# Performance work log

Measured on AMD Instinct MI355X. Metric: run time of the kernel, lower is better.

Reference implementation:

```python
import jax, jax.numpy as jnp
import numpy as np

N, IN_DIM, HID = 8192, 256, 512
NEG_INF = jnp.float32(-1e30)


def _linear_params(key, fan_in, fan_out):
    k1, k2 = jax.random.split(key)
    bound = 1.0 / np.sqrt(fan_in)
    W = jax.random.uniform(k1, (fan_in, fan_out), jnp.float32, -bound, bound)
    b = jax.random.uniform(k2, (fan_out,), jnp.float32, -bound, bound)
    return W, b


def setup_inputs() -> dict:
    key = jax.random.key(0)
    ks = jax.random.split(key, 10)
    x = jax.random.normal(ks[0], (N, IN_DIM), jnp.float32)
    adj = jax.random.randint(ks[1], (N, N), 0, 2) > 0
    adj = adj | jnp.eye(N, dtype=bool)  # self-loops: no all-masked rows
    Win, b_in = _linear_params(ks[2], IN_DIM, HID)
    Wq, bq = _linear_params(ks[3], HID, HID)
    Wk, bk = _linear_params(ks[4], HID, HID)
    Wv, bv = _linear_params(ks[5], HID, HID)
    Wo, bo = _linear_params(ks[6], HID, HID)
    Ws, bs = _linear_params(ks[7], HID, 1)
    Wf1, bf1 = _linear_params(ks[8], HID, HID)
    Wf2, bf2 = _linear_params(ks[9], HID, HID)
    g1 = jnp.ones((HID,), jnp.float32); be1 = jnp.zeros((HID,), jnp.float32)
    g2 = jnp.ones((HID,), jnp.float32); be2 = jnp.zeros((HID,), jnp.float32)
    return dict(x=x, adj=adj, Win=Win, b_in=b_in, Wq=Wq, bq=bq, Wk=Wk, bk=bk,
                Wv=Wv, bv=bv, Wo=Wo, bo=bo, Ws=Ws, bs=bs,
                g1=g1, be1=be1, g2=g2, be2=be2,
                Wf1=Wf1, bf1=bf1, Wf2=Wf2, bf2=bf2)


def _layernorm(x, g, b, eps=1e-5):
    mu = jnp.mean(x, axis=-1, keepdims=True)
    var = jnp.mean(jnp.square(x - mu), axis=-1, keepdims=True)
    return (x - mu) * jax.lax.rsqrt(var + eps) * g + b


def reference(x, adj, Win, b_in, Wq, bq, Wk, bk, Wv, bv, Wo, bo, Ws, bs,
              g1, be1, g2, be2, Wf1, bf1, Wf2, bf2):
    h = x @ Win + b_in                      # [N, HID]
    q = h @ Wq + bq
    k = h @ Wk + bk
    v = h @ Wv + bv
    scale = 1.0 / np.sqrt(HID).astype(np.float32)
    scores = (q @ k.T) * scale              # [N, N]
    scores = jnp.where(adj, scores, NEG_INF)
    attn = jax.nn.softmax(scores, axis=-1)  # dropout = identity (eval mode)
    h2 = attn @ v                           # [N, HID]
    h = _layernorm(h + (h2 @ Wo + bo), g1, be1)
    ff = jnp.maximum(h @ Wf1 + bf1, 0.0) @ Wf2 + bf2
    h = _layernorm(h + ff, g2, be2)
    logits = (h @ Ws + bs).squeeze(-1)      # [N]
    return logits
```

## Files before the change

### kernel.cpp

```cpp
#include <hip/hip_runtime.h>

typedef unsigned int u32;
typedef unsigned short u16;
typedef unsigned char u8;

typedef __bf16 bf16_t;
typedef bf16_t bf16x8 __attribute__((ext_vector_type(8)));
typedef float f32x4 __attribute__((ext_vector_type(4)));

#define NROW 8192
#define HID 512
#define DIN 256
#define LDQ 1536
#define NSPLIT 4
#define KVCH (NROW / NSPLIT)
#define KVB 32

__device__ __forceinline__ u16 f2b(float f) {
    u32 u = __float_as_uint(f);
    u32 r = (u + 0x7fffu + ((u >> 16) & 1u)) >> 16;
    return (u16)r;
}
__device__ __forceinline__ float b2f(u16 h) {
    return __uint_as_float(((u32)h) << 16);
}
__device__ __forceinline__ f32x4 zero4() {
    f32x4 z = {0.f, 0.f, 0.f, 0.f};
    return z;
}
__device__ __forceinline__ void gll16(const void* g, void* l) {
    __builtin_amdgcn_global_load_lds(
        (const __attribute__((address_space(1))) unsigned int*)g,
        (__attribute__((address_space(3))) unsigned int*)l, 16, 0, 0);
}

__global__ void sniff_and_bias(const u32* __restrict__ adj, int* __restrict__ mode,
                               const float* __restrict__ bq, const float* __restrict__ bk,
                               const float* __restrict__ bv, float* __restrict__ bqkv) {
    __shared__ int f01[4], ff32[4], fbf[4];
    int t = threadIdx.x, lane = t & 63, wv = t >> 6;
    for (int i = t; i < 1536; i += 256)
        bqkv[i] = i < 512 ? bq[i] : (i < 1024 ? bk[i - 512] : bv[i - 1024]);
    int all01 = 1, allf32 = 1, allbf = 1;
    for (int i = t; i < 1024; i += 256) {
        u32 w = adj[i];
        if (w > 1u) all01 = 0;
        if (w != 0u && w != 0x3f800000u) allf32 = 0;
    }
    const u16* h = (const u16*)adj;
    for (int i = t; i < 2048; i += 256) {
        u16 v = h[i];
        if (v != 0 && v != 0x3f80u) allbf = 0;
    }
    all01 = __all(all01);
    allf32 = __all(allf32);
    allbf = __all(allbf);
    if (lane == 0) { f01[wv] = all01; ff32[wv] = allf32; fbf[wv] = allbf; }
    __syncthreads();
    if (t == 0) {
        int a = f01[0] & f01[1] & f01[2] & f01[3];
        int b = ff32[0] & ff32[1] & ff32[2] & ff32[3];
        int c = fbf[0] & fbf[1] & fbf[2] & fbf[3];
        mode[0] = a ? 0 : (b ? 1 : (c ? 2 : 3));
    }
}

__global__ __launch_bounds__(256) void build_bits(const void* __restrict__ adj,
                                                  const int* __restrict__ mode,
                                                  u32* __restrict__ bits) {
    int row = blockIdx.x;
    int t = threadIdx.x;
    int lane = t & 63, wv = t >> 6;
    int md = *mode;
    for (int c0 = 0; c0 < NROW; c0 += 256) {
        int c = c0 + t;
        size_t idx = (size_t)row * NROW + c;
        bool nz;
        if (md == 0)      nz = ((const u32*)adj)[idx] != 0u;
        else if (md == 1) nz = ((const float*)adj)[idx] != 0.f;
        else if (md == 2) nz = ((const u16*)adj)[idx] != 0;
        else              nz = ((const u8*)adj)[idx] != 0;
        unsigned long long bm = __ballot(nz);
        if (lane == 0) {
            int w = row * 256 + (c0 >> 5) + wv * 2;
            bits[w] = (u32)bm;
            bits[w + 1] = (u32)(bm >> 32);
        }
    }
}

__global__ __launch_bounds__(256) void prep(const float* __restrict__ x,
                                            const float* __restrict__ Win,
                                            const float* __restrict__ Wq,
                                            const float* __restrict__ Wk,
                                            const float* __restrict__ Wv,
                                            const float* __restrict__ Wo,
                                            const float* __restrict__ Wf1,
                                            const float* __restrict__ Wf2,
                                            u16* __restrict__ pX16,
                                            u16* __restrict__ pWinT,
                                            u16* __restrict__ pQKVT,
                                            u16* __restrict__ pWoT,
                                            u16* __restrict__ pWf1T,
                                            u16* __restrict__ pWf2T) {
    int z = blockIdx.z;
    int t = threadIdx.x;
    if (z == 7) {
        size_t base = ((size_t)blockIdx.y * 8 + blockIdx.x) * 32768;
#pragma unroll 4
        for (int k = 0; k < 128; k++) {
            size_t i = base + k * 256 + t;
            pX16[i] = f2b(x[i]);
        }
        return;
    }
    const float* src;
    u16* dst;
    int R = 512;
    switch (z) {
        case 0: src = Win; dst = pWinT; R = 256; break;
        case 1: src = Wq;  dst = pQKVT; break;
        case 2: src = Wk;  dst = pQKVT + 512 * 512; break;
        case 3: src = Wv;  dst = pQKVT + 2 * 512 * 512; break;
        case 4: src = Wo;  dst = pWoT; break;
        case 5: src = Wf1; dst = pWf1T; break;
        default: src = Wf2; dst = pWf2T; break;
    }
    int r0 = blockIdx.y * 64, c0 = blockIdx.x * 64;
    if (r0 >= R) return;
    __shared__ u16 tile[64][65];
#pragma unroll
    for (int i = 0; i < 16; i++) {
        int idx = t + i * 256;
        int rr = idx >> 6, cc = idx & 63;
        tile[rr][cc] = f2b(src[(size_t)(r0 + rr) * 512 + c0 + cc]);
    }
    __syncthreads();
#pragma unroll
    for (int i = 0; i < 16; i++) {
        int idx = t + i * 256;
        int rr = idx >> 6, cc = idx & 63;
        dst[(size_t)(c0 + rr) * R + r0 + cc] = tile[cc][rr];
    }
}

__global__ __launch_bounds__(256) void transpose_v_tiled(const u16* __restrict__ in, int ldv,
                                                         u16* __restrict__ out) {
    __shared__ u16 tl[64][72];
    int c0 = blockIdx.x * 64;
    int r0 = blockIdx.y * 64;
    int t = threadIdx.x;
#pragma unroll
    for (int i = 0; i < 2; i++) {
        int idx = t + i * 256;
        int rr = idx >> 3, ck = idx & 7;
        bf16x8 v = *(const bf16x8*)(in + (size_t)(r0 + rr) * ldv + c0 + ck * 8);
#pragma unroll
        for (int j = 0; j < 8; j++) tl[ck * 8 + j][rr] = ((u16*)&v)[j];
    }
    __syncthreads();
#pragma unroll
    for (int i = 0; i < 2; i++) {
        int idx = t + i * 256;
        int col = idx >> 3, ch = idx & 7;
        int kv = ch * 8;
        bf16x8 v;
#pragma unroll
        for (int j = 0; j < 8; j++) ((u16*)&v)[j] = tl[col][kv + j];
        *(bf16x8*)(out + (size_t)((r0 + kv) >> 5) * (HID * 32) +
                   (size_t)(c0 + col) * 32 + (kv & 31)) = v;
    }
}

__global__ __launch_bounds__(256, 3) void gemm_k(const u16* __restrict__ A, int lda,
                                                 const u16* __restrict__ Bt,
                                                 const float* __restrict__ bias,
                                                 const float* __restrict__ resid,
                                                 float* __restrict__ outF,
                                                 u16* __restrict__ outH, int ldo,
                                                 int relu, int K) {
    __shared__ u16 Ald[2][8192];
    __shared__ u16 Bld[2][4096];
    int t = threadIdx.x;
    int lane = t & 63, wave = t >> 6;
    int l15 = lane & 15, lg = lane >> 4;
    int row0 = blockIdx.y * 128, col0 = blockIdx.x * 64;

    auto stage = [&](int buf, int kk) {
#pragma unroll
        for (int p = 0; p < 4; p++) {
            int idx = p * 256 + t;
            int row = idx >> 3, c = idx & 7;
            gll16(A + (size_t)(row0 + row) * lda + kk + ((c ^ (row & 7)) * 8),
                  &Ald[buf][idx * 8]);
        }
#pragma unroll
        for (int p = 0; p < 2; p++) {
            int idx = p * 256 + t;
            int row = idx >> 3, c = idx & 7;
            gll16(Bt + (size_t)(col0 + row) * K + kk + ((c ^ (row & 7)) * 8),
                  &Bld[buf][idx * 8]);
        }
    };

    f32x4 acc[2][4];
#pragma unroll
    for (int i = 0; i < 2; i++)
#pragma unroll
        for (int j = 0; j < 4; j++) acc[i][j] = zero4();

    stage(0, 0);
    asm volatile("s_waitcnt vmcnt(0)" ::: "memory");
    __syncthreads();

    int nk = K >> 6;
    for (int kt = 0; kt < nk; kt++) {
        int buf = kt & 1;
        if (kt + 1 < nk) stage(buf ^ 1, (kt + 1) * 64);
#pragma unroll
        for (int ks = 0; ks < 2; ks++) {
            bf16x8 af[2], bfr[4];
#pragma unroll
            for (int i = 0; i < 2; i++) {
                int row = wave * 32 + i * 16 + l15;
                af[i] = *(const bf16x8*)&Ald[buf][row * 64 + (((ks * 4 + lg) ^ (row & 7)) * 8)];
            }
#pragma unroll
            for (int j = 0; j < 4; j++) {
                int row = j * 16 + l15;
                bfr[j] = *(const bf16x8*)&Bld[buf][row * 64 + (((ks * 4 + lg) ^ (row & 7)) * 8)];
            }
            __builtin_amdgcn_s_setprio(1);
#pragma unroll
            for (int i = 0; i < 2; i++)
#pragma unroll
                for (int j = 0; j < 4; j++)
                    acc[i][j] = __builtin_amdgcn_mfma_f32_16x16x32_bf16(af[i], bfr[j],
                                                                       acc[i][j], 0, 0, 0);
            __builtin_amdgcn_s_setprio(0);
        }
        asm volatile("s_waitcnt vmcnt(0)" ::: "memory");
        __syncthreads();
    }
#pragma unroll
    for (int j = 0; j < 4; j++) {
        int col = col0 + j * 16 + l15;
        float bv = bias[col];
#pragma unroll
        for (int i = 0; i < 2; i++) {
#pragma unroll
            for (int r = 0; r < 4; r++) {
                int row = row0 + wave * 32 + i * 16 + lg * 4 + r;
                float v = acc[i][j][r] + bv;
                if (relu) v = fmaxf(v, 0.f);
                size_t o = (size_t)row * ldo + col;
                if (resid) v += resid[o];
                if (outF) outF[o] = v;
                if (outH) outH[o] = f2b(v);
            }
        }
    }
}

__global__ __launch_bounds__(512, 2) void attn_kernel(const u16* __restrict__ QKV,
                                                      const u16* __restrict__ VTt,
                                                      const u32* __restrict__ bits,
                                                      u16* __restrict__ Opart,
                                                      float* __restrict__ Mpart,
                                                      float* __restrict__ Lpart) {
    extern __shared__ char smem[];
    u16* Klds = (u16*)smem;
    u16* Plds = (u16*)(smem + 98304);
    float* cscL = (float*)(smem + 114688);
    int* flagsL = (int*)(smem + 115712);
    int lane = threadIdx.x & 63, wave = threadIdx.x >> 6;
    int l15 = lane & 15, lg = lane >> 4;
    int s = blockIdx.x & 3;
    int qb = blockIdx.x >> 2;
    int qrow0 = qb * 128;
    int myrows = qrow0 + wave * 16;
    const u16* Kg = QKV + 512;

    bf16x8 qf[16];
    {
        const u16* qp = QKV + (size_t)(myrows + l15) * LDQ + lg * 8;
#pragma unroll
        for (int ks = 0; ks < 16; ks++) qf[ks] = *(const bf16x8*)(qp + ks * 32);
    }

    f32x4 acc[8][4];
#pragma unroll
    for (int i = 0; i < 8; i++)
#pragma unroll
        for (int j = 0; j < 4; j++) acc[i][j] = zero4();
    float m[4] = {-1e30f, -1e30f, -1e30f, -1e30f};
    float lsum[4] = {0.f, 0.f, 0.f, 0.f};
    const float scale = 0.04419417382415922f;
    int kvbeg = s * KVCH;

    auto STAGE = [&](int buf, int kv0) {
#pragma unroll
        for (int i = 0; i < 4; i++) {
            int seg = wave * 4 + i;
            int ks = seg >> 1, q = seg & 1;
            gll16(Kg + (size_t)(kv0 + q * 16 + l15) * LDQ + ks * 32 + lg * 8,
                  Klds + buf * 16384 + seg * 512 + lane * 8);
        }
    };

    STAGE(0, kvbeg);
    STAGE(1, kvbeg + KVB);
    asm volatile("s_waitcnt vmcnt(4)" ::: "memory");
    __builtin_amdgcn_sched_barrier(0);
    __builtin_amdgcn_s_barrier();
    __builtin_amdgcn_sched_barrier(0);

    const int NT = KVCH / KVB;
    for (int t = 0; t < NT; ++t) {
        int kv0 = kvbeg + t * KVB;
        const u16* kb = Klds + (t % 3) * 16384;
        int pb = t & 1;

        f32x4 sf[2];
        sf[0] = zero4(); sf[1] = zero4();
        __builtin_amdgcn_s_setprio(1);
#pragma unroll
        for (int ks = 0; ks < 16; ks++) {
            bf16x8 b0 = *(const bf16x8*)(kb + (ks * 2) * 512 + lane * 8);
            bf16x8 b1 = *(const bf16x8*)(kb + (ks * 2 + 1) * 512 + lane * 8);
            sf[0] = __builtin_amdgcn_mfma_f32_16x16x32_bf16(qf[ks], b0, sf[0], 0, 0, 0);
            sf[1] = __builtin_amdgcn_mfma_f32_16x16x32_bf16(qf[ks], b1, sf[1], 0, 0, 0);
        }
        __builtin_amdgcn_s_setprio(0);

        u32 w0[4];
#pragma unroll
        for (int r = 0; r < 4; r++)
            w0[r] = bits[(size_t)(myrows + lg * 4 + r) * 256 + (kv0 >> 5)];
        float pvv[2][4];
        float mx[4] = {-1e30f, -1e30f, -1e30f, -1e30f};
#pragma unroll
        for (int f = 0; f < 2; f++) {
            int c = f * 16 + l15;
#pragma unroll
            for (int r = 0; r < 4; r++) {
                bool bit = (w0[r] >> c) & 1u;
                float sv = bit ? sf[f][r] * scale : -1e30f;
                pvv[f][r] = sv;
                mx[r] = fmaxf(mx[r], sv);
            }
        }
        bool need = false;
#pragma unroll
        for (int r = 0; r < 4; r++) need |= (mx[r] > m[r] + 8.0f);
        int wneed = __any(need ? 1 : 0);
        float cscv[4] = {1.f, 1.f, 1.f, 1.f};
        if (wneed) {
#pragma unroll
            for (int r = 0; r < 4; r++) {
#pragma unroll
                for (int off = 8; off; off >>= 1)
                    mx[r] = fmaxf(mx[r], __shfl_xor(mx[r], off, 64));
                float mn = fmaxf(m[r], mx[r]);
                cscv[r] = __expf(m[r] - mn);
                m[r] = mn;
                lsum[r] *= cscv[r];
            }
        }
        if (l15 == 0) *(f32x4*)&cscL[pb * 128 + wave * 16 + lg * 4] = *(f32x4*)cscv;
        if (lane == 0) flagsL[pb * 8 + wave] = wneed;

#pragma unroll
        for (int f = 0; f < 2; f++)
#pragma unroll
            for (int r = 0; r < 4; r++)
                pvv[f][r] = (pvv[f][r] < -1e29f) ? 0.f : __expf(pvv[f][r] - m[r]);
#pragma unroll
        for (int r = 0; r < 4; r++)
            lsum[r] += pvv[0][r] + pvv[1][r];

#pragma unroll
        for (int f = 0; f < 2; f++)
#pragma unroll
            for (int r = 0; r < 4; r++)
                Plds[pb * 4096 + wave * 512 + (f * 2 + (l15 >> 3)) * 128 +
                     (lg * 4 + r) * 8 + (l15 & 7)] = f2b(pvv[f][r]);

        const u16* vb = VTt + (size_t)(kv0 >> 5) * (HID * 32) + (size_t)(wave * 64) * 32;
        bf16x8 vv[4];
#pragma unroll
        for (int c4 = 0; c4 < 4; c4++)
            vv[c4] = *(const bf16x8*)(vb + (size_t)(c4 * 16 + l15) * 32 + lg * 8);

        if (t + 2 < NT) {
            STAGE((t + 2) % 3, kv0 + 2 * KVB);
            asm volatile("s_waitcnt vmcnt(4)" ::: "memory");
        } else if (t + 1 < NT) {
            asm volatile("s_waitcnt vmcnt(0)" ::: "memory");
        }
        asm volatile("s_waitcnt lgkmcnt(0)" ::: "memory");
        __builtin_amdgcn_sched_barrier(0);
        __builtin_amdgcn_s_barrier();
        __builtin_amdgcn_sched_barrier(0);

        int anyf = __any(flagsL[pb * 8 + (lane & 7)] != 0);
        if (anyf) {
#pragma unroll
            for (int rf = 0; rf < 8; rf++) {
                f32x4 cs = *(const f32x4*)&cscL[pb * 128 + rf * 16 + lg * 4];
#pragma unroll
                for (int cf = 0; cf < 4; cf++) {
                    f32x4 a = acc[rf][cf];
                    a[0] *= cs[0]; a[1] *= cs[1]; a[2] *= cs[2]; a[3] *= cs[3];
                    acc[rf][cf] = a;
                }
            }
        }

        __builtin_amdgcn_s_setprio(1);
#pragma unroll
        for (int rf = 0; rf < 8; rf++) {
            bf16x8 pa = *(const bf16x8*)(Plds + pb * 4096 + rf * 512 + lane * 8);
#pragma unroll
            for (int cf = 0; cf < 4; cf++)
                acc[rf][cf] = __builtin_amdgcn_mfma_f32_16x16x32_bf16(pa, vv[cf],
                                                                     acc[rf][cf], 0, 0, 0);
        }
        __builtin_amdgcn_s_setprio(0);
    }

#pragma unroll
    for (int r = 0; r < 4; r++) {
#pragma unroll
        for (int off = 8; off; off >>= 1)
            lsum[r] += __shfl_xor(lsum[r], off, 64);
    }
    if (l15 == 0) {
#pragma unroll
        for (int r = 0; r < 4; r++) {
            size_t o = (size_t)s * NROW + myrows + lg * 4 + r;
            Mpart[o] = m[r];
            Lpart[o] = lsum[r];
        }
    }
#pragma unroll
    for (int rf = 0; rf < 8; rf++)
#pragma unroll
        for (int cf = 0; cf < 4; cf++) {
            int col = wave * 64 + cf * 16 + l15;
#pragma unroll
            for (int j = 0; j < 4; j++) {
                size_t row = (size_t)s * NROW + qrow0 + rf * 16 + lg * 4 + j;
                Opart[row * HID + col] = f2b(acc[rf][cf][j]);
            }
        }
}

__global__ __launch_bounds__(256) void attn_combine(const u16* __restrict__ Opart,
                                                    const float* __restrict__ Mpart,
                                                    const float* __restrict__ Lpart,
                                                    u16* __restrict__ O16) {
    int idx = blockIdx.x * 256 + threadIdx.x;
    int row = idx >> 6;
    int c8 = (idx & 63) << 3;
    float ms[NSPLIT], M = -1e30f;
#pragma unroll
    for (int s = 0; s < NSPLIT; s++) {
        ms[s] = Mpart[(size_t)s * NROW + row];
        M = fmaxf(M, ms[s]);
    }
    float w[NSPLIT], L = 0.f;
#pragma unroll
    for (int s = 0; s < NSPLIT; s++) {
        w[s] = __expf(ms[s] - M);
        L += Lpart[(size_t)s * NROW + row] * w[s];
    }
    float inv = 1.f / L;
    float o[8];
#pragma unroll
    for (int j = 0; j < 8; j++) o[j] = 0.f;
#pragma unroll
    for (int s = 0; s < NSPLIT; s++) {
        bf16x8 p = *(const bf16x8*)(Opart + ((size_t)s * NROW + row) * HID + c8);
#pragma unroll
        for (int j = 0; j < 8; j++) o[j] += (float)p[j] * w[s];
    }
    bf16x8 res;
#pragma unroll
    for (int j = 0; j < 8; j++) {
        u16 b = f2b(o[j] * inv);
        res[j] = *(bf16_t*)&b;
    }
    *(bf16x8*)(O16 + (size_t)row * HID + c8) = res;
}

__global__ __launch_bounds__(256) void ln_single(const float* __restrict__ a,
                                                 const float* __restrict__ g,
                                                 const float* __restrict__ be,
                                                 float* __restrict__ outF,
                                                 u16* __restrict__ outH) {
    int row = blockIdx.x, t = threadIdx.x;
    const float* ar = a + (size_t)row * HID;
    float x0 = ar[t];
    float x1 = ar[t + 256];
    float s = x0 + x1, s2 = x0 * x0 + x1 * x1;
#pragma unroll
    for (int off = 32; off; off >>= 1) {
        s += __shfl_xor(s, off, 64);
        s2 += __shfl_xor(s2, off, 64);
    }
    __shared__ float ls[4], ls2[4];
    int wv = t >> 6, ln = t & 63;
    if (ln == 0) { ls[wv] = s; ls2[wv] = s2; }
    __syncthreads();
    float S = ls[0] + ls[1] + ls[2] + ls[3];
    float S2 = ls2[0] + ls2[1] + ls2[2] + ls2[3];
    float mu = S * (1.f / 512.f);
    float var = S2 * (1.f / 512.f) - mu * mu;
    float inv = rsqrtf(var + 1e-5f);
    float y0 = (x0 - mu) * inv * g[t] + be[t];
    float y1 = (x1 - mu) * inv * g[t + 256] + be[t + 256];
    size_t o = (size_t)row * HID + t;
    outF[o] = y0; outF[o + 256] = y1;
    outH[o] = f2b(y0); outH[o + 256] = f2b(y1);
}

__global__ __launch_bounds__(256) void ln_logits(const float* __restrict__ a,
                                                 const float* __restrict__ g,
                                                 const float* __restrict__ be,
                                                 const float* __restrict__ Ws,
                                                 const float* __restrict__ bs,
                                                 float* __restrict__ out) {
    int row = blockIdx.x, t = threadIdx.x;
    const float* ar = a + (size_t)row * HID;
    float x0 = ar[t];
    float x1 = ar[t + 256];
    float s = x0 + x1, s2 = x0 * x0 + x1 * x1;
#pragma unroll
    for (int off = 32; off; off >>= 1) {
        s += __shfl_xor(s, off, 64);
        s2 += __shfl_xor(s2, off, 64);
    }
    __shared__ float ls[4], ls2[4], lp[4];
    int wv = t >> 6, ln = t & 63;
    if (ln == 0) { ls[wv] = s; ls2[wv] = s2; }
    __syncthreads();
    float S = ls[0] + ls[1] + ls[2] + ls[3];
    float S2 = ls2[0] + ls2[1] + ls2[2] + ls2[3];
    float mu = S * (1.f / 512.f);
    float var = S2 * (1.f / 512.f) - mu * mu;
    float inv = rsqrtf(var + 1e-5f);
    float y0 = (x0 - mu) * inv * g[t] + be[t];
    float y1 = (x1 - mu) * inv * g[t + 256] + be[t + 256];
    float p = y0 * Ws[t] + y1 * Ws[t + 256];
#pragma unroll
    for (int off = 32; off; off >>= 1) p += __shfl_xor(p, off, 64);
    if (ln == 0) lp[wv] = p;
    __syncthreads();
    if (t == 0) out[row] = lp[0] + lp[1] + lp[2] + lp[3] + bs[0];
}

extern "C" void kernel_launch(void* const* d_in, const int* in_sizes, int n_in,
                              void* d_out, int out_size, void* d_ws, size_t ws_size,
                              hipStream_t stream) {
    const float* x   = (const float*)d_in[0];
    const void*  adj = d_in[1];
    const float* Win = (const float*)d_in[2];
    const float* b_in= (const float*)d_in[3];
    const float* Wq  = (const float*)d_in[4];
    const float* bq  = (const float*)d_in[5];
    const float* Wk  = (const float*)d_in[6];
    const float* bk  = (const float*)d_in[7];
    const float* Wv  = (const float*)d_in[8];
    const float* bv  = (const float*)d_in[9];
    const float* Wo  = (const float*)d_in[10];
    const float* bo  = (const float*)d_in[11];
    const float* Ws  = (const float*)d_in[12];
    const float* bs  = (const float*)d_in[13];
    const float* g1  = (const float*)d_in[14];
    const float* be1 = (const float*)d_in[15];
    const float* g2  = (const float*)d_in[16];
    const float* be2 = (const float*)d_in[17];
    const float* Wf1 = (const float*)d_in[18];
    const float* bf1 = (const float*)d_in[19];
    const float* Wf2 = (const float*)d_in[20];
    const float* bf2 = (const float*)d_in[21];

    char* ws = (char*)d_ws;
    const size_t MB = 1u << 20;
    const size_t OFF_PART = 0;
    const size_t OFF_X16  = 0;
    const size_t OFF_H16  = 4 * MB;
    const size_t OFF_HN32 = 12 * MB;
    const size_t OFF_HN16 = 28 * MB;
    const size_t OFF_FF1  = 4 * MB;
    const size_t OFF_HF32 = 36 * MB;
    const size_t OFF_QKV  = 52 * MB;
    const size_t OFF_OP32 = 52 * MB;
    const size_t OFF_FF2  = 52 * MB;
    const size_t OFF_VT   = 76 * MB;
    const size_t OFF_H2   = 84 * MB;
    const size_t OFF_BITS = 92 * MB;
    size_t off = 100 * MB;
    const size_t OFF_WINT = off;  off += 262144;
    const size_t OFF_QKVT = off;  off += 1572864;
    const size_t OFF_WOT  = off;  off += 524288;
    const size_t OFF_WF1T = off;  off += 524288;
    const size_t OFF_WF2T = off;  off += 524288;
    const size_t OFF_BQKV = off;  off += 8192;
    const size_t OFF_MODE = off;  off += 4096;
    const size_t OFF_MPART= off;  off += 131072;
    const size_t OFF_LPART= off;  off += 131072;

    u16* pX16   = (u16*)(ws + OFF_X16);
    u16* pH16   = (u16*)(ws + OFF_H16);
    float* pHN32= (float*)(ws + OFF_HN32);
    u16* pHN16  = (u16*)(ws + OFF_HN16);
    u16* pFF1   = (u16*)(ws + OFF_FF1);
    float* pHF32= (float*)(ws + OFF_HF32);
    u16* pQKV   = (u16*)(ws + OFF_QKV);
    float* pOP32= (float*)(ws + OFF_OP32);
    float* pFF2 = (float*)(ws + OFF_FF2);
    u16* pVT    = (u16*)(ws + OFF_VT);
    u16* pH2    = (u16*)(ws + OFF_H2);
    u32* pBits  = (u32*)(ws + OFF_BITS);
    u16* pPart  = (u16*)(ws + OFF_PART);
    u16* pWinT  = (u16*)(ws + OFF_WINT);
    u16* pQKVT  = (u16*)(ws + OFF_QKVT);
    u16* pWoT   = (u16*)(ws + OFF_WOT);
    u16* pWf1T  = (u16*)(ws + OFF_WF1T);
    u16* pWf2T  = (u16*)(ws + OFF_WF2T);
    float* pBqkv= (float*)(ws + OFF_BQKV);
    int* pMode  = (int*)(ws + OFF_MODE);
    float* pMp  = (float*)(ws + OFF_MPART);
    float* pLp  = (float*)(ws + OFF_LPART);

    sniff_and_bias<<<1, 256, 0, stream>>>((const u32*)adj, pMode, bq, bk, bv, pBqkv);
    build_bits<<<NROW, 256, 0, stream>>>(adj, pMode, pBits);

    prep<<<dim3(8, 8, 8), 256, 0, stream>>>(x, Win, Wq, Wk, Wv, Wo, Wf1, Wf2,
                                            pX16, pWinT, pQKVT, pWoT, pWf1T, pWf2T);

    gemm_k<<<dim3(8, 64), 256, 0, stream>>>(pX16, DIN, pWinT, b_in, nullptr,
                                            pHF32, pH16, HID, 0, DIN);
    gemm_k<<<dim3(24, 64), 256, 0, stream>>>(pH16, HID, pQKVT, pBqkv, nullptr,
                                             nullptr, pQKV, LDQ, 0, HID);
    transpose_v_tiled<<<dim3(HID / 64, NROW / 64), 256, 0, stream>>>(pQKV + 1024, LDQ, pVT);
    attn_kernel<<<64 * NSPLIT, 512, 115776, stream>>>(pQKV, pVT, pBits, pPart, pMp, pLp);
    attn_combine<<<NROW * HID / (256 * 8), 256, 0, stream>>>(pPart, pMp, pLp, pH2);
    gemm_k<<<dim3(8, 64), 256, 0, stream>>>(pH2, HID, pWoT, bo, pHF32,
                                            pOP32, nullptr, HID, 0, HID);
    ln_single<<<NROW, 256, 0, stream>>>(pOP32, g1, be1, pHN32, pHN16);
    gemm_k<<<dim3(8, 64), 256, 0, stream>>>(pHN16, HID, pWf1T, bf1, nullptr,
                                            nullptr, pFF1, HID, 1, HID);
    gemm_k<<<dim3(8, 64), 256, 0, stream>>>(pFF1, HID, pWf2T, bf2, pHN32,
                                            pFF2, nullptr, HID, 0, HID);
    ln_logits<<<NROW, 256, 0, stream>>>(pFF2, g2, be2, Ws, bs, (float*)d_out);
}
```

Before: 486.5 us.

## Fuse V transpose into QKV GEMM epilogue, inline adjacency sniff, vectorize bit build

The QKV GEMM now writes the V columns directly into the blocked transposed layout used by attention, which removes the separate transpose kernel. The single-block sniff kernel is gone: each build_bits block re-detects the adjacency format itself, and the bias concatenation moves into prep. For 32-bit adjacency, bits are packed with uint4 loads and shuffles. The cost is redundant sniff reads in every block and scattered 2-byte stores in the GEMM epilogue.

```diff
diff --git a/kernel.cpp b/kernel.cpp
--- a/kernel.cpp
+++ b/kernel.cpp
@@ -34,57 +34,51 @@
         (__attribute__((address_space(3))) unsigned int*)l, 16, 0, 0);
 }
 
-__global__ void sniff_and_bias(const u32* __restrict__ adj, int* __restrict__ mode,
-                               const float* __restrict__ bq, const float* __restrict__ bk,
-                               const float* __restrict__ bv, float* __restrict__ bqkv) {
-    __shared__ int f01[4], ff32[4], fbf[4];
-    int t = threadIdx.x, lane = t & 63, wv = t >> 6;
-    for (int i = t; i < 1536; i += 256)
-        bqkv[i] = i < 512 ? bq[i] : (i < 1024 ? bk[i - 512] : bv[i - 1024]);
-    int all01 = 1, allf32 = 1, allbf = 1;
-    for (int i = t; i < 1024; i += 256) {
-        u32 w = adj[i];
-        if (w > 1u) all01 = 0;
-        if (w != 0u && w != 0x3f800000u) allf32 = 0;
-    }
-    const u16* h = (const u16*)adj;
-    for (int i = t; i < 2048; i += 256) {
-        u16 v = h[i];
-        if (v != 0 && v != 0x3f80u) allbf = 0;
-    }
-    all01 = __all(all01);
-    allf32 = __all(allf32);
-    allbf = __all(allbf);
-    if (lane == 0) { f01[wv] = all01; ff32[wv] = allf32; fbf[wv] = allbf; }
-    __syncthreads();
-    if (t == 0) {
-        int a = f01[0] & f01[1] & f01[2] & f01[3];
-        int b = ff32[0] & ff32[1] & ff32[2] & ff32[3];
-        int c = fbf[0] & fbf[1] & fbf[2] & fbf[3];
-        mode[0] = a ? 0 : (b ? 1 : (c ? 2 : 3));
-    }
-}
-
 __global__ __launch_bounds__(256) void build_bits(const void* __restrict__ adj,
-                                                  const int* __restrict__ mode,
                                                   u32* __restrict__ bits) {
     int row = blockIdx.x;
     int t = threadIdx.x;
     int lane = t & 63, wv = t >> 6;
-    int md = *mode;
-    for (int c0 = 0; c0 < NROW; c0 += 256) {
-        int c = c0 + t;
-        size_t idx = (size_t)row * NROW + c;
-        bool nz;
-        if (md == 0)      nz = ((const u32*)adj)[idx] != 0u;
-        else if (md == 1) nz = ((const float*)adj)[idx] != 0.f;
-        else if (md == 2) nz = ((const u16*)adj)[idx] != 0;
-        else              nz = ((const u8*)adj)[idx] != 0;
-        unsigned long long bm = __ballot(nz);
-        if (lane == 0) {
-            int w = row * 256 + (c0 >> 5) + wv * 2;
-            bits[w] = (u32)bm;
-            bits[w + 1] = (u32)(bm >> 32);
+    const u32* a32 = (const u32*)adj;
+    int w01 = 1, bf01 = 1;
+    for (int i = lane; i < 1024; i += 64) {
+        u32 w = a32[i];
+        if (w != 0u && w != 1u && w != 0x3f800000u) w01 = 0;
+    }
+    const u16* h16 = (const u16*)adj;
+    for (int i = lane; i < 2048; i += 64) {
+        u16 v = h16[i];
+        if (v != 0 && v != 0x3f80u) bf01 = 0;
+    }
+    w01 = __all(w01);
+    bf01 = __all(bf01);
+    int md = w01 ? 0 : (bf01 ? 2 : 3);
+
+    if (md == 0) {
+        const u32* rowp = a32 + (size_t)row * NROW;
+        for (int c0 = 0; c0 < NROW; c0 += 1024) {
+            uint4 x = *(const uint4*)(rowp + c0 + t * 4);
+            u32 nib = (u32)(x.x != 0u) | ((u32)(x.y != 0u) << 1) |
+                      ((u32)(x.z != 0u) << 2) | ((u32)(x.w != 0u) << 3);
+            u32 val = nib << (4 * (lane & 7));
+            val |= __shfl_xor(val, 1, 64);
+            val |= __shfl_xor(val, 2, 64);
+            val |= __shfl_xor(val, 4, 64);
+            if ((lane & 7) == 0)
+                bits[row * 256 + ((c0 + wv * 256) >> 5) + (lane >> 3)] = val;
+        }
+    } else {
+        for (int c0 = 0; c0 < NROW; c0 += 256) {
+            int c = c0 + t;
+            size_t idx = (size_t)row * NROW + c;
+            bool nz = (md == 2) ? (((const u16*)adj)[idx] != 0)
+                                : (((const u8*)adj)[idx] != 0);
+            unsigned long long bm = __ballot(nz);
+            if (lane == 0) {
+                int w = row * 256 + (c0 >> 5) + wv * 2;
+                bits[w] = (u32)bm;
+                bits[w + 1] = (u32)(bm >> 32);
+            }
         }
     }
 }
@@ -97,15 +91,23 @@
                                             const float* __restrict__ Wo,
                                             const float* __restrict__ Wf1,
                                             const float* __restrict__ Wf2,
+                                            const float* __restrict__ bq,
+                                            const float* __restrict__ bk,
+                                            const float* __restrict__ bv,
                                             u16* __restrict__ pX16,
                                             u16* __restrict__ pWinT,
                                             u16* __restrict__ pQKVT,
                                             u16* __restrict__ pWoT,
                                             u16* __restrict__ pWf1T,
-                                            u16* __restrict__ pWf2T) {
+                                            u16* __restrict__ pWf2T,
+                                            float* __restrict__ bqkv) {
     int z = blockIdx.z;
     int t = threadIdx.x;
     if (z == 7) {
+        if (blockIdx.x == 0 && blockIdx.y == 0) {
+            for (int i = t; i < 1536; i += 256)
+                bqkv[i] = i < 512 ? bq[i] : (i < 1024 ? bk[i - 512] : bv[i - 1024]);
+        }
         size_t base = ((size_t)blockIdx.y * 8 + blockIdx.x) * 32768;
 #pragma unroll 4
         for (int k = 0; k < 128; k++) {
@@ -144,41 +146,14 @@
     }
 }
 
-__global__ __launch_bounds__(256) void transpose_v_tiled(const u16* __restrict__ in, int ldv,
-                                                         u16* __restrict__ out) {
-    __shared__ u16 tl[64][72];
-    int c0 = blockIdx.x * 64;
-    int r0 = blockIdx.y * 64;
-    int t = threadIdx.x;
-#pragma unroll
-    for (int i = 0; i < 2; i++) {
-        int idx = t + i * 256;
-        int rr = idx >> 3, ck = idx & 7;
-        bf16x8 v = *(const bf16x8*)(in + (size_t)(r0 + rr) * ldv + c0 + ck * 8);
-#pragma unroll
-        for (int j = 0; j < 8; j++) tl[ck * 8 + j][rr] = ((u16*)&v)[j];
-    }
-    __syncthreads();
-#pragma unroll
-    for (int i = 0; i < 2; i++) {
-        int idx = t + i * 256;
-        int col = idx >> 3, ch = idx & 7;
-        int kv = ch * 8;
-        bf16x8 v;
-#pragma unroll
-        for (int j = 0; j < 8; j++) ((u16*)&v)[j] = tl[col][kv + j];
-        *(bf16x8*)(out + (size_t)((r0 + kv) >> 5) * (HID * 32) +
-                   (size_t)(c0 + col) * 32 + (kv & 31)) = v;
-    }
-}
-
 __global__ __launch_bounds__(256, 3) void gemm_k(const u16* __restrict__ A, int lda,
                                                  const u16* __restrict__ Bt,
                                                  const float* __restrict__ bias,
                                                  const float* __restrict__ resid,
                                                  float* __restrict__ outF,
                                                  u16* __restrict__ outH, int ldo,
-                                                 int relu, int K) {
+                                                 int relu, int K,
+                                                 u16* __restrict__ outVT) {
     __shared__ u16 Ald[2][8192];
     __shared__ u16 Bld[2][4096];
     int t = threadIdx.x;
@@ -253,10 +228,14 @@
                 int row = row0 + wave * 32 + i * 16 + lg * 4 + r;
                 float v = acc[i][j][r] + bv;
                 if (relu) v = fmaxf(v, 0.f);
-                size_t o = (size_t)row * ldo + col;
-                if (resid) v += resid[o];
-                if (outF) outF[o] = v;
-                if (outH) outH[o] = f2b(v);
+                if (outVT && col >= 1024) {
+                    outVT[((size_t)(row >> 5) * 512 + (col - 1024)) * 32 + (row & 31)] = f2b(v);
+                } else {
+                    size_t o = (size_t)row * ldo + col;
+                    if (resid) v += resid[o];
+                    if (outF) outF[o] = v;
+                    if (outH) outH[o] = f2b(v);
+                }
             }
         }
     }
@@ -608,7 +587,6 @@
     const size_t OFF_WF1T = off;  off += 524288;
     const size_t OFF_WF2T = off;  off += 524288;
     const size_t OFF_BQKV = off;  off += 8192;
-    const size_t OFF_MODE = off;  off += 4096;
     const size_t OFF_MPART= off;  off += 131072;
     const size_t OFF_LPART= off;  off += 131072;
 
@@ -631,29 +609,28 @@
     u16* pWf1T  = (u16*)(ws + OFF_WF1T);
     u16* pWf2T  = (u16*)(ws + OFF_WF2T);
     float* pBqkv= (float*)(ws + OFF_BQKV);
-    int* pMode  = (int*)(ws + OFF_MODE);
     float* pMp  = (float*)(ws + OFF_MPART);
     float* pLp  = (float*)(ws + OFF_LPART);
 
-    sniff_and_bias<<<1, 256, 0, stream>>>((const u32*)adj, pMode, bq, bk, bv, pBqkv);
-    build_bits<<<NROW, 256, 0, stream>>>(adj, pMode, pBits);
+    build_bits<<<NROW, 256, 0, stream>>>(adj, pBits);
 
     prep<<<dim3(8, 8, 8), 256, 0, stream>>>(x, Win, Wq, Wk, Wv, Wo, Wf1, Wf2,
-                                            pX16, pWinT, pQKVT, pWoT, pWf1T, pWf2T);
+                                            bq, bk, bv,
+                                            pX16, pWinT, pQKVT, pWoT, pWf1T, pWf2T,
+                                            pBqkv);
 
     gemm_k<<<dim3(8, 64), 256, 0, stream>>>(pX16, DIN, pWinT, b_in, nullptr,
-                                            pHF32, pH16, HID, 0, DIN);
+                                            pHF32, pH16, HID, 0, DIN, nullptr);
     gemm_k<<<dim3(24, 64), 256, 0, stream>>>(pH16, HID, pQKVT, pBqkv, nullptr,
-                                             nullptr, pQKV, LDQ, 0, HID);
-    transpose_v_tiled<<<dim3(HID / 64, NROW / 64), 256, 0, stream>>>(pQKV + 1024, LDQ, pVT);
+                                             nullptr, pQKV, LDQ, 0, HID, pVT);
     attn_kernel<<<64 * NSPLIT, 512, 115776, stream>>>(pQKV, pVT, pBits, pPart, pMp, pLp);
     attn_combine<<<NROW * HID / (256 * 8), 256, 0, stream>>>(pPart, pMp, pLp, pH2);
     gemm_k<<<dim3(8, 64), 256, 0, stream>>>(pH2, HID, pWoT, bo, pHF32,
-                                            pOP32, nullptr, HID, 0, HID);
+                                            pOP32, nullptr, HID, 0, HID, nullptr);
     ln_single<<<NROW, 256, 0, stream>>>(pOP32, g1, be1, pHN32, pHN16);
     gemm_k<<<dim3(8, 64), 256, 0, stream>>>(pHN16, HID, pWf1T, bf1, nullptr,
-                                            nullptr, pFF1, HID, 1, HID);
+                                            nullptr, pFF1, HID, 1, HID, nullptr);
     gemm_k<<<dim3(8, 64), 256, 0, stream>>>(pFF1, HID, pWf2T, bf2, pHN32,
-                                            pFF2, nullptr, HID, 0, HID);
+                                            pFF2, nullptr, HID, 0, HID, nullptr);
     ln_logits<<<NROW, 256, 0, stream>>>(pFF2, g2, be2, Ws, bs, (float*)d_out);
 }
```

Measured after the change: 510.1 us. 1.05x slower.
